# Optimization experiments

Measured on AMD Instinct MI355X. Metric: run time of the kernel, lower is better.

## Reference

```python
import jax, jax.numpy as jnp
import numpy as np

TEMPERATURE = 0.07
N_CLASSES = 100


def setup_inputs() -> dict:
    key = jax.random.key(0)
    k1, k2 = jax.random.split(key)
    N, D = 8192, 128
    emb = jax.random.normal(k1, (N, D), dtype=jnp.float32)
    # unit-normalize so exp(sim / temperature) stays finite in fp32
    emb = emb / jnp.linalg.norm(emb, axis=1, keepdims=True)
    labels = jax.random.randint(k2, (N,), 0, N_CLASSES, dtype=jnp.int64)
    return {"embeddings": emb, "labels": labels}


def reference(embeddings, labels):
    N = embeddings.shape[0]
    dt = embeddings.dtype
    # [N, N] similarity
    sim = jnp.matmul(embeddings, embeddings.T) / TEMPERATURE
    off_diag = 1.0 - jnp.eye(N, dtype=dt)
    pos_mask = (labels[:, None] == labels[None, :]).astype(dt) * off_diag
    exp_sim = jnp.exp(sim) * off_diag  # diagonal zeroed
    positive_sum = jnp.sum(exp_sim * pos_mask, axis=1)
    total_sum = jnp.sum(exp_sim, axis=1)
    loss = -jnp.log(positive_sum / (total_sum + 1e-8) + 1e-8)
    valid = pos_mask.sum(axis=1) > 0
    cnt = jnp.sum(valid.astype(dt))
    mean_loss = jnp.where(
        cnt > 0,
        jnp.sum(jnp.where(valid, loss, jnp.zeros_like(loss))) / jnp.maximum(cnt, 1.0),
        jnp.asarray(0.0, dtype=dt),
    )
    return mean_loss
```

## Files before the change

### kernel.cpp

```cpp
#include <hip/hip_runtime.h>

#define N 8192
#define D 128
#define SCALE_A 20.6098592f
#define NBX 64
#define NBY 8
#define NBLK (NBX * NBY)

using short8  = __attribute__((ext_vector_type(8))) short;
using float4v = __attribute__((ext_vector_type(4))) float;

#if __has_builtin(__builtin_amdgcn_exp2f)
#define EXP2(x) __builtin_amdgcn_exp2f(x)
#else
#define EXP2(x) __expf((x) * 0.69314718f)
#endif

static __device__ inline unsigned int f2bf(float f) {
    union { float f; unsigned int u; } x;
    x.f = f;
    unsigned int u = x.u;
    return (u + 0x7FFFu + ((u >> 16) & 1u)) >> 16;
}

__global__ __launch_bounds__(256) void cl_prep(
    const float* __restrict__ emb, unsigned short* __restrict__ bfB,
    unsigned short* __restrict__ bfA, float* __restrict__ tot,
    int* __restrict__ ticket)
{
    const int t = blockIdx.x * 256 + threadIdx.x;
    const float* p = emb + (size_t)t * 16;
    uint4 ob[2], oa[2];
    #pragma unroll
    for (int h = 0; h < 2; ++h) {
        float4v f0 = *(const float4v*)(p + h * 8);
        float4v f1 = *(const float4v*)(p + h * 8 + 4);
        ob[h].x = f2bf(f0[0]) | (f2bf(f0[1]) << 16);
        ob[h].y = f2bf(f0[2]) | (f2bf(f0[3]) << 16);
        ob[h].z = f2bf(f1[0]) | (f2bf(f1[1]) << 16);
        ob[h].w = f2bf(f1[2]) | (f2bf(f1[3]) << 16);
        oa[h].x = f2bf(f0[0] * SCALE_A) | (f2bf(f0[1] * SCALE_A) << 16);
        oa[h].y = f2bf(f0[2] * SCALE_A) | (f2bf(f0[3] * SCALE_A) << 16);
        oa[h].z = f2bf(f1[0] * SCALE_A) | (f2bf(f1[1] * SCALE_A) << 16);
        oa[h].w = f2bf(f1[2] * SCALE_A) | (f2bf(f1[3] * SCALE_A) << 16);
    }
    ((uint4*)bfB)[t * 2]     = ob[0];
    ((uint4*)bfB)[t * 2 + 1] = ob[1];
    ((uint4*)bfA)[t * 2]     = oa[0];
    ((uint4*)bfA)[t * 2 + 1] = oa[1];
    if (t < 2 * N) tot[t] = 0.f;
    if (t == 0) *ticket = 0;
}

__global__ __launch_bounds__(256, 2) void cl_main(
    const unsigned short* __restrict__ bfA, const unsigned short* __restrict__ bfB,
    const int* __restrict__ labels,
    float* __restrict__ tot, float* __restrict__ pos,
    int* __restrict__ ticket, float* __restrict__ out)
{
    __shared__ uint4 ldsB[128 * 16];
    __shared__ float sred[2][4];
    __shared__ int s_ticket;

    const int tid  = threadIdx.x;
    const int lane = tid & 63;
    const int wave = tid >> 6;
    const int q    = lane >> 4;
    const int c    = lane & 15;
    const int rw   = blockIdx.x * 128 + wave * 32;

    short8 afrag[2][4];
    int rowlab[2][4];
    #pragma unroll
    for (int tr = 0; tr < 2; ++tr) {
        const int arow = rw + tr * 16 + c;
        #pragma unroll
        for (int ks = 0; ks < 4; ++ks)
            afrag[tr][ks] = *(const short8*)(bfA + (size_t)arow * D + ks * 32 + q * 8);
        #pragma unroll
        for (int reg = 0; reg < 4; ++reg)
            rowlab[tr][reg] = labels[rw + tr * 16 + q * 4 + reg];
    }

    float tot_a[2][4] = {{0.f,0.f,0.f,0.f},{0.f,0.f,0.f,0.f}};
    float pos_a[2][4] = {{0.f,0.f,0.f,0.f},{0.f,0.f,0.f,0.f}};

    for (int it = 0; it < 8; ++it) {
        const int cbase = blockIdx.y * 1024 + it * 128;

        const uint4* bfB4 = (const uint4*)bfB;
        #pragma unroll
        for (int i = 0; i < 8; ++i) {
            const int g     = tid + i * 256;
            const int brow  = g >> 4;
            const int chunk = g & 15;
            uint4 u = bfB4[(size_t)(cbase + brow) * 16 + chunk];
            ldsB[brow * 16 + (chunk ^ (brow & 15))] = u;
        }
        int collab[8];
        #pragma unroll
        for (int tc = 0; tc < 8; ++tc) collab[tc] = labels[cbase + tc * 16 + c];
        __syncthreads();

        float4v acc[2][8];
        #pragma unroll
        for (int tr = 0; tr < 2; ++tr)
            #pragma unroll
            for (int tc = 0; tc < 8; ++tc) {
                float4v z = {0.f, 0.f, 0.f, 0.f};
                acc[tr][tc] = z;
            }

        const short8* ldsS = (const short8*)ldsB;
        #pragma unroll
        for (int ks = 0; ks < 4; ++ks) {
            const short8* pk = ldsS + c * 16 + ((ks * 4 + q) ^ c);
            #pragma unroll
            for (int tc = 0; tc < 8; ++tc) {
                short8 b = pk[tc * 256];
                #pragma unroll
                for (int tr = 0; tr < 2; ++tr)
                    acc[tr][tc] = __builtin_amdgcn_mfma_f32_16x16x32_bf16(
                        afrag[tr][ks], b, acc[tr][tc], 0, 0, 0);
            }
        }

        #pragma unroll
        for (int tr = 0; tr < 2; ++tr) {
            const int rtile = rw + tr * 16;
            #pragma unroll
            for (int tc = 0; tc < 8; ++tc) {
                const bool diag_tile = (rtile == cbase + tc * 16);
                const int lc = collab[tc];
                #pragma unroll
                for (int reg = 0; reg < 4; ++reg) {
                    float v = EXP2(acc[tr][tc][reg]);
                    if (diag_tile && (q * 4 + reg) == c) v = 0.f;
                    tot_a[tr][reg] += v;
                    if (rowlab[tr][reg] == lc) pos_a[tr][reg] += v;
                }
            }
        }
        __syncthreads();
    }

    #pragma unroll
    for (int tr = 0; tr < 2; ++tr)
        #pragma unroll
        for (int reg = 0; reg < 4; ++reg) {
            float t = tot_a[tr][reg];
            float p = pos_a[tr][reg];
            #pragma unroll
            for (int m = 1; m < 16; m <<= 1) {
                t += __shfl_xor(t, m, 64);
                p += __shfl_xor(p, m, 64);
            }
            if (c == 0) {
                const int r = rw + tr * 16 + q * 4 + reg;
                atomicAdd(&tot[r], t);
                atomicAdd(&pos[r], p);
            }
        }

    asm volatile("s_waitcnt vmcnt(0)" ::: "memory");
    __syncthreads();
    if (tid == 0)
        s_ticket = __hip_atomic_fetch_add(ticket, 1, __ATOMIC_RELAXED,
                                          __HIP_MEMORY_SCOPE_AGENT);
    __syncthreads();
    if (s_ticket != NBLK - 1) return;

    float lsum = 0.f, lcnt = 0.f;
    #pragma unroll 4
    for (int i = tid; i < N; i += 256) {
        const float t = __hip_atomic_load(&tot[i], __ATOMIC_RELAXED,
                                          __HIP_MEMORY_SCOPE_AGENT);
        const float p = __hip_atomic_load(&pos[i], __ATOMIC_RELAXED,
                                          __HIP_MEMORY_SCOPE_AGENT);
        const float loss = -__logf(p / (t + 1e-8f) + 1e-8f);
        if (p > 0.f) { lsum += loss; lcnt += 1.f; }
    }
    #pragma unroll
    for (int m = 1; m < 64; m <<= 1) {
        lsum += __shfl_xor(lsum, m, 64);
        lcnt += __shfl_xor(lcnt, m, 64);
    }
    if (lane == 0) { sred[0][wave] = lsum; sred[1][wave] = lcnt; }
    __syncthreads();
    if (tid == 0) {
        const float s = sred[0][0] + sred[0][1] + sred[0][2] + sred[0][3];
        const float n = sred[1][0] + sred[1][1] + sred[1][2] + sred[1][3];
        out[0] = (n > 0.f) ? s / fmaxf(n, 1.f) : 0.f;
    }
}

extern "C" void kernel_launch(void* const* d_in, const int* in_sizes, int n_in,
                              void* d_out, int out_size, void* d_ws, size_t ws_size,
                              hipStream_t stream) {
    const float* emb  = (const float*)d_in[0];
    const int* labels = (const int*)d_in[1];
    unsigned short* bfB = (unsigned short*)d_ws;
    unsigned short* bfA = bfB + (size_t)N * D;
    float* tot    = (float*)(bfA + (size_t)N * D);
    float* pos    = tot + N;
    int*   ticket = (int*)(pos + N);

    cl_prep<<<256, 256, 0, stream>>>(emb, bfB, bfA, tot, ticket);
    cl_main<<<dim3(NBX, NBY), 256, 0, stream>>>(bfA, bfB, labels, tot, pos,
                                                ticket, (float*)d_out);
}
```

Measured before the change: 91.98 us.

## Drop LDS staging of B; use 64x64 per-wave tiles loaded directly from global

Each wave now computes a 64x64 tile: four row tiles against four column tiles, with waves paired over row groups and column halves. B fragments are loaded straight from global/L2 into registers instead of being staged through swizzled LDS, which removes both __syncthreads per iteration. The square tile gives better operand reuse per MFMA, but it raises register pressure (16 accumulators plus 16 A fragments) and exposes global-load latency with no LDS double-buffering.

```diff
diff --git a/kernel.cpp b/kernel.cpp
--- a/kernel.cpp
+++ b/kernel.cpp
@@ -58,78 +58,73 @@
     float* __restrict__ tot, float* __restrict__ pos,
     int* __restrict__ ticket, float* __restrict__ out)
 {
-    __shared__ uint4 ldsB[128 * 16];
     __shared__ float sred[2][4];
     __shared__ int s_ticket;
 
-    const int tid  = threadIdx.x;
-    const int lane = tid & 63;
-    const int wave = tid >> 6;
-    const int q    = lane >> 4;
-    const int c    = lane & 15;
-    const int rw   = blockIdx.x * 128 + wave * 32;
-
-    short8 afrag[2][4];
-    int rowlab[2][4];
-    #pragma unroll
-    for (int tr = 0; tr < 2; ++tr) {
-        const int arow = rw + tr * 16 + c;
+    const int tid   = threadIdx.x;
+    const int lane  = tid & 63;
+    const int wave  = tid >> 6;
+    const int q     = lane >> 4;
+    const int c     = lane & 15;
+    const int rgrp  = wave >> 1;
+    const int chalf = wave & 1;
+    const int rowbase = blockIdx.x * 128 + rgrp * 64;
+
+    short8 afrag[4][4];
+    int rowlab[4][4];
+    #pragma unroll
+    for (int tr = 0; tr < 4; ++tr) {
+        const int arow = rowbase + tr * 16 + c;
         #pragma unroll
         for (int ks = 0; ks < 4; ++ks)
             afrag[tr][ks] = *(const short8*)(bfA + (size_t)arow * D + ks * 32 + q * 8);
         #pragma unroll
         for (int reg = 0; reg < 4; ++reg)
-            rowlab[tr][reg] = labels[rw + tr * 16 + q * 4 + reg];
-    }
-
-    float tot_a[2][4] = {{0.f,0.f,0.f,0.f},{0.f,0.f,0.f,0.f}};
-    float pos_a[2][4] = {{0.f,0.f,0.f,0.f},{0.f,0.f,0.f,0.f}};
+            rowlab[tr][reg] = labels[rowbase + tr * 16 + q * 4 + reg];
+    }
+
+    float tot_a[4][4], pos_a[4][4];
+    #pragma unroll
+    for (int tr = 0; tr < 4; ++tr)
+        #pragma unroll
+        for (int reg = 0; reg < 4; ++reg) { tot_a[tr][reg] = 0.f; pos_a[tr][reg] = 0.f; }
 
     for (int it = 0; it < 8; ++it) {
-        const int cbase = blockIdx.y * 1024 + it * 128;
-
-        const uint4* bfB4 = (const uint4*)bfB;
-        #pragma unroll
-        for (int i = 0; i < 8; ++i) {
-            const int g     = tid + i * 256;
-            const int brow  = g >> 4;
-            const int chunk = g & 15;
-            uint4 u = bfB4[(size_t)(cbase + brow) * 16 + chunk];
-            ldsB[brow * 16 + (chunk ^ (brow & 15))] = u;
-        }
-        int collab[8];
-        #pragma unroll
-        for (int tc = 0; tc < 8; ++tc) collab[tc] = labels[cbase + tc * 16 + c];
-        __syncthreads();
-
-        float4v acc[2][8];
-        #pragma unroll
-        for (int tr = 0; tr < 2; ++tr)
-            #pragma unroll
-            for (int tc = 0; tc < 8; ++tc) {
+        const int cbase = blockIdx.y * 1024 + it * 128 + chalf * 64;
+
+        int collab[4];
+        #pragma unroll
+        for (int tc = 0; tc < 4; ++tc) collab[tc] = labels[cbase + tc * 16 + c];
+
+        float4v acc[4][4];
+        #pragma unroll
+        for (int tr = 0; tr < 4; ++tr)
+            #pragma unroll
+            for (int tc = 0; tc < 4; ++tc) {
                 float4v z = {0.f, 0.f, 0.f, 0.f};
                 acc[tr][tc] = z;
             }
 
-        const short8* ldsS = (const short8*)ldsB;
         #pragma unroll
         for (int ks = 0; ks < 4; ++ks) {
-            const short8* pk = ldsS + c * 16 + ((ks * 4 + q) ^ c);
-            #pragma unroll
-            for (int tc = 0; tc < 8; ++tc) {
-                short8 b = pk[tc * 256];
+            short8 bfr[4];
+            #pragma unroll
+            for (int tc = 0; tc < 4; ++tc)
+                bfr[tc] = *(const short8*)(bfB + (size_t)(cbase + tc * 16 + c) * D
+                                           + ks * 32 + q * 8);
+            #pragma unroll
+            for (int tc = 0; tc < 4; ++tc)
                 #pragma unroll
-                for (int tr = 0; tr < 2; ++tr)
+                for (int tr = 0; tr < 4; ++tr)
                     acc[tr][tc] = __builtin_amdgcn_mfma_f32_16x16x32_bf16(
-                        afrag[tr][ks], b, acc[tr][tc], 0, 0, 0);
-            }
+                        afrag[tr][ks], bfr[tc], acc[tr][tc], 0, 0, 0);
         }
 
         #pragma unroll
-        for (int tr = 0; tr < 2; ++tr) {
-            const int rtile = rw + tr * 16;
-            #pragma unroll
-            for (int tc = 0; tc < 8; ++tc) {
+        for (int tr = 0; tr < 4; ++tr) {
+            const int rtile = rowbase + tr * 16;
+            #pragma unroll
+            for (int tc = 0; tc < 4; ++tc) {
                 const bool diag_tile = (rtile == cbase + tc * 16);
                 const int lc = collab[tc];
                 #pragma unroll
@@ -141,11 +136,10 @@
                 }
             }
         }
-        __syncthreads();
-    }
-
-    #pragma unroll
-    for (int tr = 0; tr < 2; ++tr)
+    }
+
+    #pragma unroll
+    for (int tr = 0; tr < 4; ++tr)
         #pragma unroll
         for (int reg = 0; reg < 4; ++reg) {
             float t = tot_a[tr][reg];
@@ -156,7 +150,7 @@
                 p += __shfl_xor(p, m, 64);
             }
             if (c == 0) {
-                const int r = rw + tr * 16 + q * 4 + reg;
+                const int r = rowbase + tr * 16 + q * 4 + reg;
                 atomicAdd(&tot[r], t);
                 atomicAdd(&pos[r], p);
             }
```

Measured after the change: 107.0 us. 1.16x slower.

## Exploit similarity symmetry: compute upper-triangular tiles and scatter column sums

Applied to the files above, without the earlier changes.

Since the similarity matrix is symmetric, the kernel launches one block per upper-triangular 128x128 tile pair (2080 blocks) instead of covering the full matrix. Each off-diagonal tile contributes row sums for its rows and, through a cross-quad shuffle reduction, column sums for its columns via extra atomics. This roughly halves the MFMA and exp work. In exchange it adds more atomic traffic, a triangular index decode per block, and removes the per-block loop that amortized the A-fragment loads.

```diff
diff --git a/kernel.cpp b/kernel.cpp
--- a/kernel.cpp
+++ b/kernel.cpp
@@ -3,9 +3,7 @@
 #define N 8192
 #define D 128
 #define SCALE_A 20.6098592f
-#define NBX 64
-#define NBY 8
-#define NBLK (NBX * NBY)
+#define NBLK 2080
 
 using short8  = __attribute__((ext_vector_type(8))) short;
 using float4v = __attribute__((ext_vector_type(4))) float;
@@ -67,7 +65,17 @@
     const int wave = tid >> 6;
     const int q    = lane >> 4;
     const int c    = lane & 15;
-    const int rw   = blockIdx.x * 128 + wave * 32;
+
+    const int t = blockIdx.x;
+    int bi = (int)((129.0f - sqrtf(16641.0f - 8.0f * (float)t)) * 0.5f);
+    bi = bi < 0 ? 0 : (bi > 63 ? 63 : bi);
+    while (bi > 0 && 64 * bi - bi * (bi - 1) / 2 > t) --bi;
+    while (64 * (bi + 1) - (bi + 1) * bi / 2 <= t) ++bi;
+    const int bj   = bi + (t - (64 * bi - bi * (bi - 1) / 2));
+    const bool diag = (bi == bj);
+    const int rbase = bi * 128;
+    const int cbase = bj * 128;
+    const int rw    = rbase + wave * 32;
 
     short8 afrag[2][4];
     int rowlab[2][4];
@@ -82,12 +90,7 @@
             rowlab[tr][reg] = labels[rw + tr * 16 + q * 4 + reg];
     }
 
-    float tot_a[2][4] = {{0.f,0.f,0.f,0.f},{0.f,0.f,0.f,0.f}};
-    float pos_a[2][4] = {{0.f,0.f,0.f,0.f},{0.f,0.f,0.f,0.f}};
-
-    for (int it = 0; it < 8; ++it) {
-        const int cbase = blockIdx.y * 1024 + it * 128;
-
+    {
         const uint4* bfB4 = (const uint4*)bfB;
         #pragma unroll
         for (int i = 0; i < 8; ++i) {
@@ -97,68 +100,82 @@
             uint4 u = bfB4[(size_t)(cbase + brow) * 16 + chunk];
             ldsB[brow * 16 + (chunk ^ (brow & 15))] = u;
         }
-        int collab[8];
-        #pragma unroll
-        for (int tc = 0; tc < 8; ++tc) collab[tc] = labels[cbase + tc * 16 + c];
-        __syncthreads();
-
-        float4v acc[2][8];
-        #pragma unroll
-        for (int tr = 0; tr < 2; ++tr)
+    }
+    int collab[8];
+    #pragma unroll
+    for (int tc = 0; tc < 8; ++tc) collab[tc] = labels[cbase + tc * 16 + c];
+    __syncthreads();
+
+    float4v acc[2][8];
+    #pragma unroll
+    for (int tr = 0; tr < 2; ++tr)
+        #pragma unroll
+        for (int tc = 0; tc < 8; ++tc) {
+            float4v z = {0.f, 0.f, 0.f, 0.f};
+            acc[tr][tc] = z;
+        }
+    const short8* ldsS = (const short8*)ldsB;
+    #pragma unroll
+    for (int ks = 0; ks < 4; ++ks) {
+        const short8* pk = ldsS + c * 16 + ((ks * 4 + q) ^ c);
+        #pragma unroll
+        for (int tc = 0; tc < 8; ++tc) {
+            short8 b = pk[tc * 256];
             #pragma unroll
-            for (int tc = 0; tc < 8; ++tc) {
-                float4v z = {0.f, 0.f, 0.f, 0.f};
-                acc[tr][tc] = z;
-            }
-
-        const short8* ldsS = (const short8*)ldsB;
-        #pragma unroll
-        for (int ks = 0; ks < 4; ++ks) {
-            const short8* pk = ldsS + c * 16 + ((ks * 4 + q) ^ c);
+            for (int tr = 0; tr < 2; ++tr)
+                acc[tr][tc] = __builtin_amdgcn_mfma_f32_16x16x32_bf16(
+                    afrag[tr][ks], b, acc[tr][tc], 0, 0, 0);
+        }
+    }
+
+    float tot_a[2][4] = {{0.f,0.f,0.f,0.f},{0.f,0.f,0.f,0.f}};
+    float pos_a[2][4] = {{0.f,0.f,0.f,0.f},{0.f,0.f,0.f,0.f}};
+    #pragma unroll
+    for (int tc = 0; tc < 8; ++tc) {
+        const int lc = collab[tc];
+        const int ctile = cbase + tc * 16;
+        float colt = 0.f, colp = 0.f;
+        #pragma unroll
+        for (int tr = 0; tr < 2; ++tr) {
+            const bool diag_tile = diag && (rw + tr * 16 == ctile);
             #pragma unroll
-            for (int tc = 0; tc < 8; ++tc) {
-                short8 b = pk[tc * 256];
-                #pragma unroll
-                for (int tr = 0; tr < 2; ++tr)
-                    acc[tr][tc] = __builtin_amdgcn_mfma_f32_16x16x32_bf16(
-                        afrag[tr][ks], b, acc[tr][tc], 0, 0, 0);
-            }
-        }
-
-        #pragma unroll
-        for (int tr = 0; tr < 2; ++tr) {
-            const int rtile = rw + tr * 16;
-            #pragma unroll
-            for (int tc = 0; tc < 8; ++tc) {
-                const bool diag_tile = (rtile == cbase + tc * 16);
-                const int lc = collab[tc];
-                #pragma unroll
-                for (int reg = 0; reg < 4; ++reg) {
-                    float v = EXP2(acc[tr][tc][reg]);
-                    if (diag_tile && (q * 4 + reg) == c) v = 0.f;
-                    tot_a[tr][reg] += v;
-                    if (rowlab[tr][reg] == lc) pos_a[tr][reg] += v;
-                }
-            }
-        }
-        __syncthreads();
+            for (int reg = 0; reg < 4; ++reg) {
+                float v = EXP2(acc[tr][tc][reg]);
+                if (diag_tile && (q * 4 + reg) == c) v = 0.f;
+                const bool m = (rowlab[tr][reg] == lc);
+                tot_a[tr][reg] += v;
+                if (m) pos_a[tr][reg] += v;
+                colt += v;
+                if (m) colp += v;
+            }
+        }
+        if (!diag) {
+            colt += __shfl_xor(colt, 16, 64);
+            colt += __shfl_xor(colt, 32, 64);
+            colp += __shfl_xor(colp, 16, 64);
+            colp += __shfl_xor(colp, 32, 64);
+            if (q == 0) {
+                atomicAdd(&tot[ctile + c], colt);
+                atomicAdd(&pos[ctile + c], colp);
+            }
+        }
     }
 
     #pragma unroll
     for (int tr = 0; tr < 2; ++tr)
         #pragma unroll
         for (int reg = 0; reg < 4; ++reg) {
-            float t = tot_a[tr][reg];
-            float p = pos_a[tr][reg];
+            float tt = tot_a[tr][reg];
+            float pp = pos_a[tr][reg];
             #pragma unroll
             for (int m = 1; m < 16; m <<= 1) {
-                t += __shfl_xor(t, m, 64);
-                p += __shfl_xor(p, m, 64);
+                tt += __shfl_xor(tt, m, 64);
+                pp += __shfl_xor(pp, m, 64);
             }
             if (c == 0) {
                 const int r = rw + tr * 16 + q * 4 + reg;
-                atomicAdd(&tot[r], t);
-                atomicAdd(&pos[r], p);
+                atomicAdd(&tot[r], tt);
+                atomicAdd(&pos[r], pp);
             }
         }
 
@@ -173,12 +190,12 @@
     float lsum = 0.f, lcnt = 0.f;
     #pragma unroll 4
     for (int i = tid; i < N; i += 256) {
-        const float t = __hip_atomic_load(&tot[i], __ATOMIC_RELAXED,
-                                          __HIP_MEMORY_SCOPE_AGENT);
-        const float p = __hip_atomic_load(&pos[i], __ATOMIC_RELAXED,
-                                          __HIP_MEMORY_SCOPE_AGENT);
-        const float loss = -__logf(p / (t + 1e-8f) + 1e-8f);
-        if (p > 0.f) { lsum += loss; lcnt += 1.f; }
+        const float tt = __hip_atomic_load(&tot[i], __ATOMIC_RELAXED,
+                                           __HIP_MEMORY_SCOPE_AGENT);
+        const float pp = __hip_atomic_load(&pos[i], __ATOMIC_RELAXED,
+                                           __HIP_MEMORY_SCOPE_AGENT);
+        const float loss = -__logf(pp / (tt + 1e-8f) + 1e-8f);
+        if (pp > 0.f) { lsum += loss; lcnt += 1.f; }
     }
     #pragma unroll
     for (int m = 1; m < 64; m <<= 1) {
@@ -206,6 +223,6 @@
     int*   ticket = (int*)(pos + N);
 
     cl_prep<<<256, 256, 0, stream>>>(emb, bfB, bfA, tot, ticket);
-    cl_main<<<dim3(NBX, NBY), 256, 0, stream>>>(bfA, bfB, labels, tot, pos,
-                                                ticket, (float*)d_out);
-}
+    cl_main<<<NBLK, 256, 0, stream>>>(bfA, bfB, labels, tot, pos,
+                                      ticket, (float*)d_out);
+}
```

Result: slower. 116.8 us (+27.0%).
